# Performance work log

Measured on AMD Instinct MI355X. Metric: run time of the kernel, lower is better.

Reference implementation:

```python
import jax, jax.numpy as jnp
import numpy as np

DIM = 128
K = 4
B, H, W = 2, 256, 256
DEFORM_WEIGHT = 0.3


def conv2d(x, w, b, pad):
    # x [B,C,H,W], w [O,I,kh,kw], stride 1
    y = jax.lax.conv_general_dilated(
        x, w, (1, 1), [(pad, pad), (pad, pad)],
        dimension_numbers=('NCHW', 'OIHW', 'NCHW'))
    return y + b[None, :, None, None]


def gelu(x):
    return jax.nn.gelu(x, approximate=False)  # torch nn.GELU default (erf)


def grid_sample_k(feat, grid):
    """Bilinear grid_sample, padding_mode='border', align_corners=True.
    feat: [B,C,H,W]; grid: [B,K,H,W,2] (x,y) in [-1,1]. Returns [B,C,K,H,W]."""
    Bn, C, Hh, Ww = feat.shape
    px = (grid[..., 0] + 1.0) * 0.5 * (Ww - 1)
    py = (grid[..., 1] + 1.0) * 0.5 * (Hh - 1)
    px = jnp.clip(px, 0.0, Ww - 1)
    py = jnp.clip(py, 0.0, Hh - 1)
    x0 = jnp.floor(px).astype(jnp.int32)
    y0 = jnp.floor(py).astype(jnp.int32)
    x1 = jnp.minimum(x0 + 1, Ww - 1)
    y1 = jnp.minimum(y0 + 1, Hh - 1)
    wx = (px - x0)[:, None]  # [B,1,K,H,W]
    wy = (py - y0)[:, None]
    featf = feat.reshape(Bn, C, Hh * Ww)

    def gather(yi, xi):
        idx = (yi * Ww + xi).reshape(Bn, -1)  # [B, K*H*W]
        g = jax.vmap(lambda f, i: f[:, i])(featf, idx)  # [B,C,K*H*W]
        return g.reshape(Bn, C, *yi.shape[1:])

    v00 = gather(y0, x0)
    v01 = gather(y0, x1)
    v10 = gather(y1, x0)
    v11 = gather(y1, x1)
    return (v00 * (1 - wx) * (1 - wy) + v01 * wx * (1 - wy)
            + v10 * (1 - wx) * wy + v11 * wx * wy)


def setup_inputs() -> dict:
    key = jax.random.key(0)
    ks = jax.random.split(key, 16)
    nrm = lambda k, shape, s: jax.random.normal(k, shape, dtype=jnp.float32) * s
    return {
        'query_feat': jax.random.normal(ks[0], (B, DIM, H, W), dtype=jnp.float32),
        'key_feat': jax.random.normal(ks[1], (B, DIM, H, W), dtype=jnp.float32),
        # offset_net: Conv(dim,dim,3) -> GELU -> Conv(dim,2K,3); small scale keeps offsets sane
        'ow1': nrm(ks[2], (DIM, DIM, 3, 3), 0.02), 'ob1': jnp.zeros((DIM,), jnp.float32),
        'ow2': nrm(ks[3], (2 * K, DIM, 3, 3), 0.01), 'ob2': jnp.zeros((2 * K,), jnp.float32),
        # weight_net: Conv(dim,dim//4,3) -> GELU -> Conv(dim//4,K,1)
        'ww1': nrm(ks[4], (DIM // 4, DIM, 3, 3), 0.05), 'wb1': jnp.zeros((DIM // 4,), jnp.float32),
        'ww2': nrm(ks[5], (K, DIM // 4, 1, 1), 0.05), 'wb2': jnp.zeros((K,), jnp.float32),
        # fusion_conv: Conv(dim,dim,1) -> GELU -> Conv(dim,dim,1)
        'fw1': nrm(ks[6], (DIM, DIM, 1, 1), 0.05), 'fb1': jnp.zeros((DIM,), jnp.float32),
        'fw2': nrm(ks[7], (DIM, DIM, 1, 1), 0.05), 'fb2': jnp.zeros((DIM,), jnp.float32),
    }


def reference(query_feat, key_feat, ow1, ob1, ow2, ob2, ww1, wb1, ww2, wb2,
              fw1, fb1, fw2, fb2):
    offsets = conv2d(gelu(conv2d(query_feat, ow1, ob1, 1)), ow2, ob2, 1)  # [B,2K,H,W]
    wlog = conv2d(gelu(conv2d(query_feat, ww1, wb1, 1)), ww2, wb2, 0)     # [B,K,H,W]
    Bn, C, Hh, Ww = key_feat.shape
    Kp = wlog.shape[1]
    off = offsets.reshape(Bn, Kp, 2, Hh, Ww).transpose(0, 1, 3, 4, 2)  # [B,K,H,W,2]
    gy, gx = jnp.meshgrid(jnp.linspace(-1.0, 1.0, Hh),
                          jnp.linspace(-1.0, 1.0, Ww), indexing='ij')
    base = jnp.stack([gx, gy], axis=-1).astype(off.dtype)  # [H,W,2] (x,y)
    scale = jnp.array([Ww / 2.0, Hh / 2.0], dtype=off.dtype)
    grid = jnp.clip(base + off / scale, -1.0, 1.0)  # [B,K,H,W,2]
    sampled = grid_sample_k(key_feat, grid)  # [B,C,K,H,W]
    wsoft = jax.nn.softmax(wlog, axis=1)[:, None]  # [B,1,K,H,W]
    agg = (sampled * wsoft).sum(axis=2)  # [B,C,H,W]
    fused = conv2d(gelu(conv2d(agg, fw1, fb1, 0)), fw2, fb2, 0)
    return query_feat + fused * DEFORM_WEIGHT
```

## Files before the change

kernel.cpp:

```cpp
#include <hip/hip_runtime.h>
#include <hip/hip_fp16.h>

typedef unsigned short u16;
typedef __attribute__((ext_vector_type(8))) short bf16x8;
typedef __attribute__((ext_vector_type(4))) float f32x4;

constexpr int B_ = 2, C_ = 128, H_ = 256, W_ = 256, P_ = H_ * W_;
constexpr int HP_ = 258, WP_ = 258;

union HU { __half2 h; unsigned int u; };

__device__ __forceinline__ float bf2f(u16 u) {
  union { unsigned int i; float f; } v; v.i = ((unsigned int)u) << 16; return v.f;
}
__device__ __forceinline__ u16 f2bf(float f) {
  union { float f; unsigned int i; } v; v.f = f;
  return (u16)((v.i + 0x7fffu + ((v.i >> 16) & 1u)) >> 16);
}
__device__ __forceinline__ float gelu_f(float x) {
  float u = x * (1.5957691216057308f + 0.071354816272f * x * x);
  return x / (1.0f + __expf(-u));
}

__device__ __forceinline__ void async16(const u16* g, u16* l) {
  __builtin_amdgcn_global_load_lds(
      (const __attribute__((address_space(1))) unsigned int*)g,
      (__attribute__((address_space(3))) unsigned int*)l, 16, 0, 0);
}

__global__ __launch_bounds__(256) void prologue(
    const float* __restrict__ q, const float* __restrict__ key,
    const float* __restrict__ ow1, const float* __restrict__ ow2,
    const float* __restrict__ ww1, const float* __restrict__ fw1,
    const float* __restrict__ fw2,
    u16* __restrict__ qpad, u16* __restrict__ keyn, u16* __restrict__ t1pad,
    u16* __restrict__ wb) {
  __shared__ u16 l[64 * 66];
  const int id = blockIdx.x, tid = threadIdx.x;
  if (id < 8192) {
    int z = id >> 10, r = id & 1023;
    int bx = r & 3, by = r >> 2;
    const float* in; u16* out; int OW, opad;
    if (z < 4) { in = q; out = qpad; OW = WP_; opad = 1; }
    else { z -= 4; in = key; out = keyn; OW = W_; opad = 0; }
    int b = z >> 1, c0 = (z & 1) * 64;
    int h = by, w0 = bx * 64;
    for (int it = 0; it < 16; ++it) {
      int lin = it * 256 + tid;
      int c = lin >> 6, w = lin & 63;
      l[c * 66 + w] = f2bf(in[(((size_t)b * C_ + c0 + c) * H_ + h) * W_ + w0 + w]);
    }
    __syncthreads();
    int OH = (opad ? HP_ : H_);
    for (int it = 0; it < 16; ++it) {
      int lin = it * 256 + tid;
      int w = lin >> 6, c = lin & 63;
      out[(((size_t)b * OH + h + opad) * OW + (w0 + w + opad)) * C_ + c0 + c] = l[c * 66 + w];
    }
  } else if (id < 10256) {
    int j = id - 8192;
    u16* buf = (j < 1032) ? qpad : t1pad;
    int idx = ((j < 1032) ? j : j - 1032) * 256 + tid;
    int c = idx & 127;
    int t = idx >> 7;
    int pos = t % 258;
    int side = (t / 258) & 3;
    int b = t / (258 * 4);
    int h, w;
    if (side == 0) { h = 0; w = pos; }
    else if (side == 1) { h = 257; w = pos; }
    else if (side == 2) { h = pos; w = 0; }
    else { h = pos; w = 257; }
    buf[(((size_t)b * HP_ + h) * WP_ + w) * C_ + c] = 0;
  } else {
    int idx = (id - 10256) * 256 + tid;
    float v;
    if (idx < 184320) {
      int e = idx & 7, lr = (idx >> 3) & 15, kb = (idx >> 7) & 3;
      int t = idx >> 9;
      int g = t % 10, u = t / 10;
      int cq = u & 3, tap = u >> 2;
      int ci = cq * 32 + kb * 8 + e, co = g * 16 + lr;
      v = (co < 128) ? ow1[(co * 128 + ci) * 9 + tap]
                     : ww1[((co - 128) * 128 + ci) * 9 + tap];
    } else if (idx < 202752) {
      int j = idx - 184320;
      int e = j & 7, lr = (j >> 3) & 15, kb = (j >> 7) & 3;
      int cq = (j >> 9) & 3, tap = j >> 11;
      int ci = cq * 32 + kb * 8 + e, co = lr;
      v = (co < 8) ? ow2[(co * 128 + ci) * 9 + tap] : 0.0f;
    } else if (idx < 219136) {
      v = fw1[idx - 202752];
    } else {
      v = fw2[idx - 219136];
    }
    wb[idx] = f2bf(v);
  }
}

__global__ __launch_bounds__(512, 4) void conv3_big(
    const u16* __restrict__ A, const u16* __restrict__ Wf,
    const float* __restrict__ bias1, const float* __restrict__ bias2,
    u16* __restrict__ outb, u16* __restrict__ outw) {
  constexpr int RPX = 36, ROWU = RPX * 32;
  __shared__ __align__(16) u16 As[6 * ROWU];
  const int tid = threadIdx.x, lane = tid & 63, wave = tid >> 6;
  const int id = blockIdx.x;
  const int s = id >> 3;
  const int h0 = (((id & 7) << 3) | (s & 7)) << 2;
  const int w0 = ((s >> 3) & 7) << 5;
  const int b = s >> 6;
  const int wr = wave >> 1, wc = wave & 1;
  const int wn = wc * 80;
  const int lr = lane & 15, kq = lane >> 4;
  const int gbase = wn >> 4;

  int preA[2][3];
#pragma unroll
  for (int i = 0; i < 2; i++)
#pragma unroll
    for (int kx = 0; kx < 3; kx++) {
      int pxv = i * 16 + lr + kx;
      preA[i][kx] = (pxv * 4 + (kq ^ ((pxv >> 1) & 3))) * 8;
    }

  f32x4 acc[2][5];
#pragma unroll
  for (int i = 0; i < 2; i++)
#pragma unroll
    for (int j = 0; j < 5; j++) { f32x4 z = {0.f, 0.f, 0.f, 0.f}; acc[i][j] = z; }

  for (int cq = 0; cq < 4; ++cq) {
    const int ci0 = cq * 32;
    __syncthreads();
    for (int i = tid; i < 864; i += 512) {
      int ry = i / 144;
      int rem = i - ry * 144;
      int px = rem >> 2, c8 = rem & 3;
      int g = c8 ^ ((px >> 1) & 3);
      async16(A + ((size_t)(b * HP_ + h0 + ry) * WP_ + (w0 + px)) * 128 + ci0 + g * 8,
              As + i * 8);
    }
    __syncthreads();
#pragma unroll
    for (int tap = 0; tap < 9; ++tap) {
      const int ky = tap / 3, kx = tap % 3;
      bf16x8 bfr[5], af[2];
#pragma unroll
      for (int j = 0; j < 5; ++j)
        bfr[j] = *(const bf16x8*)&Wf[(size_t)((((tap * 4 + cq) * 10 + gbase + j) * 4 + kq) * 16 + lr) * 8];
#pragma unroll
      for (int i = 0; i < 2; ++i)
        af[i] = *(const bf16x8*)&As[(wr + ky) * ROWU + preA[i][kx]];
#pragma unroll
      for (int i = 0; i < 2; i++)
#pragma unroll
        for (int j = 0; j < 5; j++)
          acc[i][j] = __builtin_amdgcn_mfma_f32_16x16x32_bf16(af[i], bfr[j], acc[i][j], 0, 0, 0);
    }
  }

  const int h = h0 + wr;
#pragma unroll
  for (int i = 0; i < 2; i++) {
#pragma unroll
    for (int j = 0; j < 5; j++) {
      const int co = wn + j * 16 + lr;
#pragma unroll
      for (int r = 0; r < 4; r++) {
        const int w = w0 + i * 16 + kq * 4 + r;
        float v = acc[i][j][r];
        if (co < 128) {
          v = gelu_f(v + bias1[co]);
          outb[(((size_t)b * HP_ + h + 1) * WP_ + (w + 1)) * 128 + co] = f2bf(v);
        } else {
          v = gelu_f(v + bias2[co - 128]);
          outw[((size_t)b * P_ + (size_t)h * W_ + w) * 32 + (co - 128)] = f2bf(v);
        }
      }
    }
  }
}

__global__ __launch_bounds__(256) void conv_off(
    const u16* __restrict__ A, const u16* __restrict__ Wf,
    const float* __restrict__ bias,
    const u16* __restrict__ w1b, const float* __restrict__ ww2,
    const float* __restrict__ wb2, uint4* __restrict__ desc) {
  constexpr int RPX = 66, ROWU = RPX * 32;
  __shared__ __align__(16) u16 As[6 * ROWU];
  float* off_lds = (float*)As;
  const int tid = threadIdx.x, lane = tid & 63, wave = tid >> 6;
  const int id = blockIdx.x;
  const int s = id >> 3;
  const int h0 = (((id & 7) << 3) | (s & 7)) << 2;
  const int w0 = ((s >> 3) & 3) << 6;
  const int b = s >> 5;
  const int lr = lane & 15, kq = lane >> 4;

  int preA[4][3];
#pragma unroll
  for (int i = 0; i < 4; i++)
#pragma unroll
    for (int kx = 0; kx < 3; kx++) {
      int pxv = i * 16 + lr + kx;
      preA[i][kx] = (pxv * 4 + (kq ^ ((pxv >> 1) & 3))) * 8;
    }

  f32x4 acc[4];
#pragma unroll
  for (int i = 0; i < 4; i++) { f32x4 z = {0.f, 0.f, 0.f, 0.f}; acc[i] = z; }

  for (int cq = 0; cq < 4; ++cq) {
    const int ci0 = cq * 32;
    __syncthreads();
    for (int i = tid; i < 1584; i += 256) {
      int ry = i / 264;
      int rem = i - ry * 264;
      int px = rem >> 2, c8 = rem & 3;
      int g = c8 ^ ((px >> 1) & 3);
      async16(A + ((size_t)(b * HP_ + h0 + ry) * WP_ + (w0 + px)) * 128 + ci0 + g * 8,
              As + i * 8);
    }
    __syncthreads();
#pragma unroll
    for (int tap = 0; tap < 9; ++tap) {
      const int ky = tap / 3, kx = tap % 3;
      bf16x8 bw = *(const bf16x8*)&Wf[(size_t)(((tap * 4 + cq) * 4 + kq) * 16 + lr) * 8];
      bf16x8 af[4];
#pragma unroll
      for (int i = 0; i < 4; ++i)
        af[i] = *(const bf16x8*)&As[(wave + ky) * ROWU + preA[i][kx]];
#pragma unroll
      for (int i = 0; i < 4; i++)
        acc[i] = __builtin_amdgcn_mfma_f32_16x16x32_bf16(af[i], bw, acc[i], 0, 0, 0);
    }
  }

  __syncthreads();
#pragma unroll
  for (int i = 0; i < 4; i++) {
#pragma unroll
    for (int r = 0; r < 4; r++) {
      if (lr < 8) {
        int px = i * 16 + (lane >> 4) * 4 + r;
        off_lds[(wave * 64 + px) * 9 + lr] = acc[i][r] + bias[lr];
      }
    }
  }
  __syncthreads();

  const int pp = tid;
  const int h = h0 + (pp >> 6), w = w0 + (pp & 63);
  const int pix = b * P_ + h * W_ + w;
  const u16* wp = w1b + (size_t)pix * 32;
  float f[32];
#pragma unroll
  for (int i = 0; i < 32; i += 2) {
    unsigned u = *(const unsigned*)&wp[i];
    f[i] = bf2f((u16)u); f[i + 1] = bf2f((u16)(u >> 16));
  }
  float lg[4];
#pragma unroll
  for (int k = 0; k < 4; k++) {
    float sacc = wb2[k];
#pragma unroll
    for (int i = 0; i < 32; i++) sacc = fmaf(ww2[k * 32 + i], f[i], sacc);
    lg[k] = sacc;
  }
  float mx = fmaxf(fmaxf(lg[0], lg[1]), fmaxf(lg[2], lg[3]));
  float e[4], sum = 0.f;
#pragma unroll
  for (int k = 0; k < 4; k++) { e[k] = __expf(lg[k] - mx); sum += e[k]; }
  const float inv = 1.0f / sum;
#pragma unroll
  for (int k = 0; k < 4; k++) {
    float ox = off_lds[pp * 9 + 2 * k], oy = off_lds[pp * 9 + 2 * k + 1];
    float gx = (2.0f * w / 255.0f - 1.0f) + ox * (1.0f / 128.0f);
    float gy = (2.0f * h / 255.0f - 1.0f) + oy * (1.0f / 128.0f);
    gx = fminf(fmaxf(gx, -1.f), 1.f);
    gy = fminf(fmaxf(gy, -1.f), 1.f);
    float px = fminf(fmaxf((gx + 1.f) * 127.5f, 0.f), 255.f);
    float py = fminf(fmaxf((gy + 1.f) * 127.5f, 0.f), 255.f);
    int x0 = (int)px, y0 = (int)py;
    int x1 = min(x0 + 1, 255), y1 = min(y0 + 1, 255);
    float wx = px - x0, wy = py - y0;
    float wk = e[k] * inv;
    float w00 = (1.f - wx) * (1.f - wy) * wk, w01 = wx * (1.f - wy) * wk;
    float w10 = (1.f - wx) * wy * wk,         w11 = wx * wy * wk;
    HU t01, t23;
    t01.h = __floats2half2_rn(w00, w01);
    t23.h = __floats2half2_rn(w10, w11);
    uint4 d;
    d.x = (unsigned)(y0 * 256 + x0) | ((unsigned)(x1 - x0) << 16) | ((unsigned)(y1 - y0) << 17);
    d.y = t01.u; d.z = t23.u; d.w = 0;
    desc[(size_t)pix * 4 + k] = d;
  }
}

__global__ __launch_bounds__(256) void sampler(
    const uint4* __restrict__ desc, const u16* __restrict__ keyn, u16* __restrict__ agg) {
  const int tid = threadIdx.x, lane = tid & 63, wv = tid >> 6;
  const int pix = blockIdx.x * 4 + wv;
  const int b = pix >> 16;
  const u16* kb = keyn + (size_t)b * (P_ * C_) + 2 * lane;
  float a0 = 0.f, a1 = 0.f;
#pragma unroll
  for (int k = 0; k < 4; ++k) {
    uint4 d = desc[(size_t)pix * 4 + k];
    const int boff = (int)(d.x & 0xFFFFu) << 7;
    const int o01 = (int)((d.x >> 16) & 1u) << 7;
    const int o10 = (int)((d.x >> 17) & 1u) << 15;
    const u16* c0 = kb + boff;
    unsigned u00 = *(const unsigned*)(c0);
    unsigned u01 = *(const unsigned*)(c0 + o01);
    unsigned u10 = *(const unsigned*)(c0 + o10);
    unsigned u11 = *(const unsigned*)(c0 + o10 + o01);
    HU t01, t23; t01.u = d.y; t23.u = d.z;
    float2 wA = __half22float2(t01.h);
    float2 wB = __half22float2(t23.h);
    a0 = fmaf(wA.x, bf2f((u16)u00), a0);
    a0 = fmaf(wA.y, bf2f((u16)u01), a0);
    a0 = fmaf(wB.x, bf2f((u16)u10), a0);
    a0 = fmaf(wB.y, bf2f((u16)u11), a0);
    a1 = fmaf(wA.x, bf2f((u16)(u00 >> 16)), a1);
    a1 = fmaf(wA.y, bf2f((u16)(u01 >> 16)), a1);
    a1 = fmaf(wB.x, bf2f((u16)(u10 >> 16)), a1);
    a1 = fmaf(wB.y, bf2f((u16)(u11 >> 16)), a1);
  }
  unsigned outu = ((unsigned)f2bf(a1) << 16) | (unsigned)f2bf(a0);
  *(unsigned*)&agg[(size_t)pix * C_ + 2 * lane] = outu;
}

__global__ __launch_bounds__(512, 4) void conv_fuse(
    const u16* __restrict__ Aagg, const u16* __restrict__ W1, const u16* __restrict__ W2,
    const float* __restrict__ b1, const float* __restrict__ b2,
    const float* __restrict__ resid, float* __restrict__ out) {
  __shared__ __align__(16) u16 SM[16384];
  __shared__ __align__(16) u16 T2[128 * 136];
  u16* As = SM;
  u16* Bs = SM + 8192;
  const int tid = threadIdx.x, lane = tid & 63, wave = tid >> 6;
  const int h = blockIdx.y, w0 = blockIdx.x * 128;
  const int b = blockIdx.z;
  const int wr = wave >> 1, wc = wave & 1;
  const int wm = wr * 32, wn = wc * 64;
  const int lr = lane & 15, kq = lane >> 4;
  const int sw = lr & 7;

  f32x4 acc[2][4];
#pragma unroll
  for (int i = 0; i < 2; i++)
#pragma unroll
    for (int j = 0; j < 4; j++) { f32x4 z = {0.f, 0.f, 0.f, 0.f}; acc[i][j] = z; }

  for (int c = 0; c < 2; ++c) {
    const int ci0 = c << 6;
    const u16* Ab = Aagg + (((size_t)b * H_ + h) * W_ + w0) * 128 + ci0;
    const u16* Wb = W1 + ci0;
    __syncthreads();
    for (int i = tid; i < 128 * 8; i += 512) {
      int r = i >> 3, cb = i & 7;
      async16(Ab + r * 128 + ((cb ^ (r & 7)) << 3), As + i * 8);
    }
    for (int i = tid; i < 128 * 8; i += 512) {
      int r = i >> 3, cb = i & 7;
      async16(Wb + r * 128 + ((cb ^ (r & 7)) << 3), Bs + i * 8);
    }
    __syncthreads();
#pragma unroll
    for (int ks = 0; ks < 2; ++ks) {
      const int kb = ks * 4 + kq;
      bf16x8 af[2], bfr[4];
#pragma unroll
      for (int i = 0; i < 2; i++)
        af[i] = *(const bf16x8*)&As[(wm + i * 16 + lr) * 64 + ((kb ^ sw) << 3)];
#pragma unroll
      for (int j = 0; j < 4; j++)
        bfr[j] = *(const bf16x8*)&Bs[(wn + j * 16 + lr) * 64 + ((kb ^ sw) << 3)];
#pragma unroll
      for (int i = 0; i < 2; i++)
#pragma unroll
        for (int j = 0; j < 4; j++)
          acc[i][j] = __builtin_amdgcn_mfma_f32_16x16x32_bf16(af[i], bfr[j], acc[i][j], 0, 0, 0);
    }
  }

#pragma unroll
  for (int i = 0; i < 2; i++)
#pragma unroll
    for (int j = 0; j < 4; j++) {
      const int co = wn + j * 16 + lr;
#pragma unroll
      for (int r = 0; r < 4; r++) {
        const int px = wm + i * 16 + kq * 4 + r;
        T2[px * 136 + co] = f2bf(gelu_f(acc[i][j][r] + b1[co]));
      }
    }
  __syncthreads();
  for (int i = tid; i < 2048; i += 512) {
    int r = i >> 4, sl = i & 15;
    int g = sl ^ (r & 7);
    async16(W2 + r * 128 + g * 8, SM + i * 8);
  }
  __syncthreads();

#pragma unroll
  for (int i = 0; i < 2; i++)
#pragma unroll
    for (int j = 0; j < 4; j++) { f32x4 z = {0.f, 0.f, 0.f, 0.f}; acc[i][j] = z; }
#pragma unroll
  for (int ks = 0; ks < 4; ++ks) {
    const int kc = ks * 4 + kq;
    bf16x8 af[2], bfr[4];
#pragma unroll
    for (int i = 0; i < 2; i++)
      af[i] = *(const bf16x8*)&T2[(wm + i * 16 + lr) * 136 + kc * 8];
#pragma unroll
    for (int j = 0; j < 4; j++) {
      int rr = wn + j * 16 + lr;
      bfr[j] = *(const bf16x8*)&SM[rr * 128 + (kc ^ (rr & 7)) * 8];
    }
#pragma unroll
    for (int i = 0; i < 2; i++)
#pragma unroll
      for (int j = 0; j < 4; j++)
        acc[i][j] = __builtin_amdgcn_mfma_f32_16x16x32_bf16(af[i], bfr[j], acc[i][j], 0, 0, 0);
  }

#pragma unroll
  for (int i = 0; i < 2; i++) {
#pragma unroll
    for (int j = 0; j < 4; j++) {
      const int co = wn + j * 16 + lr;
      const int w = w0 + wm + i * 16 + kq * 4;
      size_t idx = ((size_t)b * 128 + co) * (size_t)P_ + (size_t)h * W_ + w;
      float4 rv = *(const float4*)&resid[idx];
      float bi = b2[co];
      float4 ov;
      ov.x = rv.x + 0.3f * (acc[i][j][0] + bi);
      ov.y = rv.y + 0.3f * (acc[i][j][1] + bi);
      ov.z = rv.z + 0.3f * (acc[i][j][2] + bi);
      ov.w = rv.w + 0.3f * (acc[i][j][3] + bi);
      *(float4*)&out[idx] = ov;
    }
  }
}

extern "C" void kernel_launch(void* const* d_in, const int* in_sizes, int n_in,
                              void* d_out, int out_size, void* d_ws, size_t ws_size,
                              hipStream_t stream) {
  (void)in_sizes; (void)n_in; (void)out_size; (void)ws_size;
  const float* q   = (const float*)d_in[0];
  const float* key = (const float*)d_in[1];
  const float* ow1 = (const float*)d_in[2];
  const float* ob1 = (const float*)d_in[3];
  const float* ow2 = (const float*)d_in[4];
  const float* ob2 = (const float*)d_in[5];
  const float* ww1 = (const float*)d_in[6];
  const float* wb1 = (const float*)d_in[7];
  const float* ww2 = (const float*)d_in[8];
  const float* wb2 = (const float*)d_in[9];
  const float* fw1 = (const float*)d_in[10];
  const float* fb1 = (const float*)d_in[11];
  const float* fw2 = (const float*)d_in[12];
  const float* fb2 = (const float*)d_in[13];
  float* out = (float*)d_out;
  char* ws = (char*)d_ws;

  u16* qpad  = (u16*)(ws);
  u16* t1pad = (u16*)(ws + 34080768);
  u16* keyn  = (u16*)(ws + 68161536);
  u16* w1b   = (u16*)(ws + 101715968);
  u16* wbuf  = (u16*)(ws + 110104576);
  uint4* desc = (uint4*)ws;
  u16* agg = t1pad;

  prologue<<<11176, 256, 0, stream>>>(q, key, ow1, ow2, ww1, fw1, fw2,
                                      qpad, keyn, t1pad, wbuf);
  conv3_big<<<1024, 512, 0, stream>>>(qpad, wbuf, ob1, wb1, t1pad, w1b);
  conv_off<<<512, 256, 0, stream>>>(t1pad, wbuf + 184320, ob2, w1b, ww2, wb2, desc);
  sampler<<<32768, 256, 0, stream>>>(desc, keyn, agg);
  conv_fuse<<<dim3(2, 256, 2), 512, 0, stream>>>(agg, wbuf + 202752, wbuf + 219136,
                                                 fb1, fb2, q, out);
}
```

Before: 355.8 us.

## Double-buffer LDS input tiles in conv3_big to overlap loads with MFMA

Splits the shared input tile into two buffers. The next 32-channel slice is now loaded asynchronously while MFMAs run on the current one. Global and LDS offsets are computed once up front instead of inside each loop iteration, and one barrier per iteration is removed. This doubles the LDS footprint per block, which could limit occupancy, and it relies on the barrier waiting for the async loads to finish.

```diff
diff --git a/kernel.cpp b/kernel.cpp
--- a/kernel.cpp
+++ b/kernel.cpp
@@ -103,7 +103,7 @@
     const float* __restrict__ bias1, const float* __restrict__ bias2,
     u16* __restrict__ outb, u16* __restrict__ outw) {
   constexpr int RPX = 36, ROWU = RPX * 32;
-  __shared__ __align__(16) u16 As[6 * ROWU];
+  __shared__ __align__(16) u16 As[2][6 * ROWU];
   const int tid = threadIdx.x, lane = tid & 63, wave = tid >> 6;
   const int id = blockIdx.x;
   const int s = id >> 3;
@@ -124,24 +124,46 @@
       preA[i][kx] = (pxv * 4 + (kq ^ ((pxv >> 1) & 3))) * 8;
     }
 
+  size_t soff0, soff1;
+  int doff0, doff1;
+  const bool has2 = (tid + 512 < 864);
+  {
+    int i = tid;
+    int ry = i / 144;
+    int rem = i - ry * 144;
+    int px = rem >> 2, c8 = rem & 3;
+    int g = c8 ^ ((px >> 1) & 3);
+    soff0 = ((size_t)(b * HP_ + h0 + ry) * WP_ + (w0 + px)) * 128 + g * 8;
+    doff0 = i * 8;
+  }
+  {
+    int i = (tid + 512 < 864) ? tid + 512 : tid;
+    int ry = i / 144;
+    int rem = i - ry * 144;
+    int px = rem >> 2, c8 = rem & 3;
+    int g = c8 ^ ((px >> 1) & 3);
+    soff1 = ((size_t)(b * HP_ + h0 + ry) * WP_ + (w0 + px)) * 128 + g * 8;
+    doff1 = i * 8;
+  }
+
   f32x4 acc[2][5];
 #pragma unroll
   for (int i = 0; i < 2; i++)
 #pragma unroll
     for (int j = 0; j < 5; j++) { f32x4 z = {0.f, 0.f, 0.f, 0.f}; acc[i][j] = z; }
 
+  async16(A + soff0, As[0] + doff0);
+  if (has2) async16(A + soff1, As[0] + doff1);
+  __syncthreads();
+
   for (int cq = 0; cq < 4; ++cq) {
-    const int ci0 = cq * 32;
-    __syncthreads();
-    for (int i = tid; i < 864; i += 512) {
-      int ry = i / 144;
-      int rem = i - ry * 144;
-      int px = rem >> 2, c8 = rem & 3;
-      int g = c8 ^ ((px >> 1) & 3);
-      async16(A + ((size_t)(b * HP_ + h0 + ry) * WP_ + (w0 + px)) * 128 + ci0 + g * 8,
-              As + i * 8);
-    }
-    __syncthreads();
+    if (cq < 3) {
+      const int ci0 = (cq + 1) * 32;
+      u16* dst = As[(cq + 1) & 1];
+      async16(A + soff0 + ci0, dst + doff0);
+      if (has2) async16(A + soff1 + ci0, dst + doff1);
+    }
+    const u16* Ac = As[cq & 1];
 #pragma unroll
     for (int tap = 0; tap < 9; ++tap) {
       const int ky = tap / 3, kx = tap % 3;
@@ -151,13 +173,14 @@
         bfr[j] = *(const bf16x8*)&Wf[(size_t)((((tap * 4 + cq) * 10 + gbase + j) * 4 + kq) * 16 + lr) * 8];
 #pragma unroll
       for (int i = 0; i < 2; ++i)
-        af[i] = *(const bf16x8*)&As[(wr + ky) * ROWU + preA[i][kx]];
+        af[i] = *(const bf16x8*)&Ac[(wr + ky) * ROWU + preA[i][kx]];
 #pragma unroll
       for (int i = 0; i < 2; i++)
 #pragma unroll
         for (int j = 0; j < 5; j++)
           acc[i][j] = __builtin_amdgcn_mfma_f32_16x16x32_bf16(af[i], bfr[j], acc[i][j], 0, 0, 0);
     }
+    if (cq < 3) __syncthreads();
   }
 
   const int h = h0 + wr;
```

Result: no change. 362.9 us (+2.0%).
